# Kernel optimization log

Hardware: AMD Instinct MI355X
Metric: run time of the kernel (lower is better)

The kernel has to match this reference:

```python
import jax, jax.numpy as jnp
import numpy as np

B, S, D = 2, 2048, 1024
H, HD = 16, 64
SCALE = HD ** -0.5  # applied TWICE (q pre-scale + inference score scale), matching the source


def setup_inputs() -> dict:
    key = jax.random.key(0)
    ks = jax.random.split(key, 6)
    std = 0.02
    return {
        "x": jax.random.normal(ks[0], (B, S, D), dtype=jnp.float32),
        "Wq": jax.random.normal(ks[1], (D, D), dtype=jnp.float32) * std,
        "Wk": jax.random.normal(ks[2], (D, D), dtype=jnp.float32) * std,
        "Wv": jax.random.normal(ks[3], (D, D), dtype=jnp.float32) * std,
        "Wo": jax.random.normal(ks[4], (D, D), dtype=jnp.float32) * std,
        "bo": jnp.zeros((D,), dtype=jnp.float32),
    }


def reference(x, Wq, Wk, Wv, Wo, bo):
    b, s, d = x.shape
    # nn.Linear: y = x @ W^T ; split heads: b s (h hd) -> b h s hd
    def split_heads(y):
        return y.reshape(b, s, H, HD).transpose(0, 2, 1, 3)

    q = split_heads(x @ Wq.T) * SCALE          # forward pre-scales q
    k = split_heads(x @ Wk.T)
    v = split_heads(x @ Wv.T)

    # inference path scales scores by SCALE again (double scaling, faithful)
    scores = jnp.einsum("bhsd,bhtd->bhst", q, k) * SCALE  # [B,H,S,S]
    causal = jnp.triu(jnp.full((s, s), -jnp.inf, dtype=scores.dtype), k=1)
    scores = scores + causal[None, None]

    # explicit stable softmax as in the source
    m = jnp.max(scores, axis=-1, keepdims=True)
    e = jnp.exp(scores - m)
    attn = e / jnp.sum(e, axis=-1, keepdims=True)

    out = jnp.einsum("bhst,bhtd->bhsd", attn, v)          # [B,H,S,HD]
    out = out.transpose(0, 2, 1, 3).reshape(b, s, d)       # b h s hd -> b s (h hd)
    return out @ Wo.T + bo
```

## Files before the change

kernel.cpp:

```cpp
#include <hip/hip_runtime.h>
#include <stdint.h>

#define S_LEN 2048
#define DMODEL 1024
#define NHEAD 16
#define HDIM 64
#define BATCH 2

typedef float f32x4 __attribute__((ext_vector_type(4)));
typedef __bf16 bf16x8 __attribute__((ext_vector_type(8)));

typedef const void __attribute__((address_space(1)))* as1_cvp;
typedef void __attribute__((address_space(3)))* as3_vp;

__device__ __forceinline__ ushort f2bf(float f) {
    union { float f; unsigned u; } v; v.f = f;
    unsigned u = v.u;
    return (ushort)((u + 0x7fffu + ((u >> 16) & 1u)) >> 16);
}

__device__ __forceinline__ void gload16(const void* g, void* l) {
    __builtin_amdgcn_global_load_lds((as1_cvp)g, (as3_vp)l, 16, 0, 0);
}

__global__ __launch_bounds__(256) void cvt_all(
    const float* __restrict__ x,  const float* __restrict__ wq,
    const float* __restrict__ wk, const float* __restrict__ wv,
    const float* __restrict__ wo,
    ushort* __restrict__ xb, ushort* __restrict__ wqkv, ushort* __restrict__ wob,
    float qscale) {
    const float* src; ushort* dst; int n; float sc = 1.0f;
    const int DD = DMODEL * DMODEL;
    switch (blockIdx.y) {
        case 0: src = x;  dst = xb;            n = BATCH * S_LEN * DMODEL; break;
        case 1: src = wq; dst = wqkv;          n = DD; sc = qscale; break;
        case 2: src = wk; dst = wqkv + DD;     n = DD; break;
        case 3: src = wv; dst = wqkv + 2 * DD; n = DD; break;
        default: src = wo; dst = wob;          n = DD; break;
    }
    const int step = gridDim.x * 256 * 8;
    for (int i = (blockIdx.x * 256 + threadIdx.x) * 8; i < n; i += step) {
        float4 a = *(const float4*)(src + i);
        float4 b = *(const float4*)(src + i + 4);
        union { ushort us[8]; int4 v; } r;
        r.us[0] = f2bf(a.x * sc); r.us[1] = f2bf(a.y * sc);
        r.us[2] = f2bf(a.z * sc); r.us[3] = f2bf(a.w * sc);
        r.us[4] = f2bf(b.x * sc); r.us[5] = f2bf(b.y * sc);
        r.us[6] = f2bf(b.z * sc); r.us[7] = f2bf(b.w * sc);
        *(int4*)(dst + i) = r.v;
    }
}

template<int BM, int BN, bool F32OUT, bool BIAS>
__global__ __launch_bounds__(256) void gemm_nt(
    const ushort* __restrict__ A, const ushort* __restrict__ B,
    void* __restrict__ Cv, const float* __restrict__ bias,
    int M, int N, int K) {
    __shared__ ushort As[3][BM][32];
    __shared__ ushort Bs[3][BN][32];
    constexpr int MR = BM / 32, NR = BN / 32, AG = BM / 64, BG = BN / 64;
    const int tid = threadIdx.x;
    const int wave = tid >> 6, lane = tid & 63;
    const int wm = (wave >> 1) * (BM / 2), wn = (wave & 1) * (BN / 2);
    const int bm = blockIdx.x * BM, bn = blockIdx.y * BN;
    const int l15 = lane & 15, lg = lane >> 4;
    f32x4 acc[MR][NR] = {};

    const int sr = lane >> 2;
    const int ssw = (((lane & 3) ^ ((lane >> 3) & 3))) * 8;
    const ushort* gA[AG]; const ushort* gB[BG];
    int rA0[AG], rB0[BG];
#pragma unroll
    for (int i = 0; i < AG; i++) {
        rA0[i] = wave * (BM / 4) + i * 16;
        gA[i] = A + (size_t)(bm + rA0[i] + sr) * K + ssw;
    }
#pragma unroll
    for (int i = 0; i < BG; i++) {
        rB0[i] = wave * (BN / 4) + i * 16;
        gB[i] = B + (size_t)(bn + rB0[i] + sr) * K + ssw;
    }

    const int NT = K / 32;
    auto STAGE = [&](int t) {
        const int buf = t % 3;
        const int off = t * 32;
#pragma unroll
        for (int i = 0; i < AG; i++) gload16(gA[i] + off, &As[buf][rA0[i]][0]);
#pragma unroll
        for (int i = 0; i < BG; i++) gload16(gB[i] + off, &Bs[buf][rB0[i]][0]);
    };

    STAGE(0);
    if (NT > 1) STAGE(1);
    asm volatile("s_waitcnt vmcnt(4)" ::: "memory");
    asm volatile("s_barrier" ::: "memory");

    const int csA = (l15 >> 1) & 3;
    for (int t = 0; t < NT; t++) {
        const int cur = t % 3;
        if (t + 2 < NT) STAGE(t + 2);
        bf16x8 af[MR], bfr[NR];
#pragma unroll
        for (int m = 0; m < MR; m++) {
            int4 t_ = *(const int4*)&As[cur][wm + m * 16 + l15][(lg ^ csA) * 8];
            af[m] = __builtin_bit_cast(bf16x8, t_);
        }
#pragma unroll
        for (int n = 0; n < NR; n++) {
            int4 t_ = *(const int4*)&Bs[cur][wn + n * 16 + l15][(lg ^ csA) * 8];
            bfr[n] = __builtin_bit_cast(bf16x8, t_);
        }
        __builtin_amdgcn_s_setprio(1);
#pragma unroll
        for (int m = 0; m < MR; m++)
#pragma unroll
            for (int n = 0; n < NR; n++)
                acc[m][n] = __builtin_amdgcn_mfma_f32_16x16x32_bf16(af[m], bfr[n], acc[m][n], 0, 0, 0);
        __builtin_amdgcn_s_setprio(0);
        if (t + 1 < NT) {
            if (t + 2 < NT) asm volatile("s_waitcnt vmcnt(4)" ::: "memory");
            else            asm volatile("s_waitcnt vmcnt(0)" ::: "memory");
            asm volatile("s_barrier" ::: "memory");
        }
    }

    float* Cf = (float*)Cv;
    ushort* Cb = (ushort*)Cv;
#pragma unroll
    for (int m = 0; m < MR; m++) {
        const int row = bm + wm + m * 16 + lg * 4;
#pragma unroll
        for (int n = 0; n < NR; n++) {
            const int col = bn + wn + n * 16 + l15;
            const float bb = BIAS ? bias[col] : 0.0f;
#pragma unroll
            for (int j = 0; j < 4; j++) {
                float v = acc[m][n][j];
                if (F32OUT) Cf[(size_t)(row + j) * N + col] = v + bb;
                else        Cb[(size_t)(row + j) * N + col] = f2bf(v);
            }
        }
    }
}

__global__ __launch_bounds__(256) void attn_fwd(
    const ushort* __restrict__ QKV, ushort* __restrict__ Og) {
    __shared__ ushort Ks[2][64][72];
    __shared__ ushort Vt[2][64][72];
    __shared__ ushort Ps[4][16][76];
    const int tid = threadIdx.x;
    const int wave = tid >> 6, lane = tid & 63;
    const int l15 = lane & 15, lg = lane >> 4;
    const int a = blockIdx.x;
    const int qtS = a, qtB = 31 - a;
    const int bh = blockIdx.y;
    const int b = bh >> 4, h = bh & 15;
    const ushort* Qb = QKV + (size_t)b * S_LEN * 3072 + h * HDIM;
    const ushort* Kb = Qb + 1024;
    const ushort* Vb = Qb + 2048;

    const int4 onesi = {0x3F803F80, 0x3F803F80, 0x3F803F80, 0x3F803F80};
    const bf16x8 ones = __builtin_bit_cast(bf16x8, onesi);

    bf16x8 qfS[2], qfB[2];
#pragma unroll
    for (int kk = 0; kk < 2; kk++) {
        int4 tS = *(const int4*)(Qb + (size_t)(qtS * 64 + wave * 16 + l15) * 3072 + kk * 32 + lg * 8);
        qfS[kk] = __builtin_bit_cast(bf16x8, tS);
        int4 tB = *(const int4*)(Qb + (size_t)(qtB * 64 + wave * 16 + l15) * 3072 + kk * 32 + lg * 8);
        qfB[kk] = __builtin_bit_cast(bf16x8, tB);
    }

    f32x4 oS[4] = {}, oB[4] = {};
    f32x4 lS = {}, lB = {};

    const int kr = tid >> 2, kc = (tid & 3) * 8;
    const int vt_ = tid & 63, vh = (tid >> 6) * 8;
    int4 kreg0, kreg1, vreg0, vreg1;

    auto LOAD = [&](int t) {
        const ushort* kp = Kb + (size_t)(t * 64 + kr) * 3072 + kc;
        kreg0 = *(const int4*)kp;
        kreg1 = *(const int4*)(kp + 32);
        const ushort* vp = Vb + (size_t)(t * 64 + vt_) * 3072 + vh;
        vreg0 = *(const int4*)vp;
        vreg1 = *(const int4*)(vp + 32);
    };
    auto STORE = [&](int buf) {
        *(int4*)&Ks[buf][kr][kc]      = kreg0;
        *(int4*)&Ks[buf][kr][kc + 32] = kreg1;
        union { int4 v; ushort us[8]; } u0, u1;
        u0.v = vreg0; u1.v = vreg1;
#pragma unroll
        for (int j = 0; j < 8; j++) Vt[buf][vh + j][vt_] = u0.us[j];
#pragma unroll
        for (int j = 0; j < 8; j++) Vt[buf][32 + vh + j][vt_] = u1.us[j];
    };

    auto COMPUTE = [&](const bf16x8 (&qf)[2], f32x4 (&o)[4], f32x4& lacc,
                       bool diag, int cur) {
        f32x4 s[4] = {};
        __builtin_amdgcn_s_setprio(1);
#pragma unroll
        for (int kk = 0; kk < 2; kk++) {
#pragma unroll
            for (int n = 0; n < 4; n++) {
                int4 t = *(const int4*)&Ks[cur][n * 16 + l15][kk * 32 + lg * 8];
                s[n] = __builtin_amdgcn_mfma_f32_16x16x32_bf16(qf[kk], __builtin_bit_cast(bf16x8, t), s[n], 0, 0, 0);
            }
        }
        __builtin_amdgcn_s_setprio(0);
        if (diag) {
            const int qrow = wave * 16 + lg * 4;
#pragma unroll
            for (int n = 0; n < 4; n++) {
                const int tg = n * 16 + l15;
#pragma unroll
                for (int j = 0; j < 4; j++)
                    if (tg > qrow + j) s[n][j] = -1e30f;
            }
        }
#pragma unroll
        for (int n = 0; n < 4; n++)
#pragma unroll
            for (int j = 0; j < 4; j++)
                Ps[wave][lg * 4 + j][n * 16 + l15] = f2bf(__expf(s[n][j]));
        asm volatile("s_waitcnt lgkmcnt(0)" ::: "memory");
        __builtin_amdgcn_s_setprio(1);
#pragma unroll
        for (int kk = 0; kk < 2; kk++) {
            int4 tp = *(const int4*)&Ps[wave][l15][kk * 32 + lg * 8];
            bf16x8 pf = __builtin_bit_cast(bf16x8, tp);
#pragma unroll
            for (int n = 0; n < 4; n++) {
                int4 tv = *(const int4*)&Vt[cur][n * 16 + l15][kk * 32 + lg * 8];
                o[n] = __builtin_amdgcn_mfma_f32_16x16x32_bf16(pf, __builtin_bit_cast(bf16x8, tv), o[n], 0, 0, 0);
            }
            lacc = __builtin_amdgcn_mfma_f32_16x16x32_bf16(pf, ones, lacc, 0, 0, 0);
        }
        __builtin_amdgcn_s_setprio(0);
    };

    LOAD(0);
    STORE(0);
    __syncthreads();

    for (int t0 = 0; t0 <= qtB; ++t0) {
        const int cur = t0 & 1;
        if (t0 < qtB) LOAD(t0 + 1);
        COMPUTE(qfB, oB, lB, t0 == qtB, cur);
        if (t0 <= qtS) COMPUTE(qfS, oS, lS, t0 == qtS, cur);
        if (t0 < qtB) {
            STORE(cur ^ 1);
            __syncthreads();
        }
    }

#pragma unroll
    for (int j = 0; j < 4; j++) { lS[j] = 1.0f / lS[j]; lB[j] = 1.0f / lB[j]; }
#pragma unroll
    for (int n = 0; n < 4; n++)
#pragma unroll
        for (int j = 0; j < 4; j++) {
            const int qrS = qtS * 64 + wave * 16 + lg * 4 + j;
            Og[((size_t)(b * S_LEN + qrS)) * DMODEL + h * HDIM + n * 16 + l15] = f2bf(oS[n][j] * lS[j]);
            const int qrB = qtB * 64 + wave * 16 + lg * 4 + j;
            Og[((size_t)(b * S_LEN + qrB)) * DMODEL + h * HDIM + n * 16 + l15] = f2bf(oB[n][j] * lB[j]);
        }
}

extern "C" void kernel_launch(void* const* d_in, const int* in_sizes, int n_in,
                              void* d_out, int out_size, void* d_ws, size_t ws_size,
                              hipStream_t stream) {
    (void)in_sizes; (void)n_in; (void)out_size; (void)ws_size;
    const float* x  = (const float*)d_in[0];
    const float* Wq = (const float*)d_in[1];
    const float* Wk = (const float*)d_in[2];
    const float* Wv = (const float*)d_in[3];
    const float* Wo = (const float*)d_in[4];
    const float* bo = (const float*)d_in[5];
    float* out = (float*)d_out;

    const int M = BATCH * S_LEN;
    const int D = DMODEL;

    char* ws = (char*)d_ws;
    ushort* xb   = (ushort*)ws; ws += (size_t)M * D * 2;
    ushort* wqkv = (ushort*)ws; ws += (size_t)3 * D * D * 2;
    ushort* wob  = (ushort*)ws; ws += (size_t)D * D * 2;
    ushort* qkvb = (ushort*)ws; ws += (size_t)M * 3 * D * 2;
    ushort* ao   = (ushort*)ws; ws += (size_t)M * D * 2;

    const float qscale = 1.0f / 64.0f;
    cvt_all<<<dim3(512, 5), 256, 0, stream>>>(x, Wq, Wk, Wv, Wo, xb, wqkv, wob, qscale);

    gemm_nt<128, 128, false, false><<<dim3(M / 128, 3 * D / 128), 256, 0, stream>>>(
        xb, wqkv, qkvb, nullptr, M, 3 * D, D);

    attn_fwd<<<dim3(16, BATCH * NHEAD), 256, 0, stream>>>(qkvb, ao);

    gemm_nt<64, 128, true, true><<<dim3(M / 64, D / 128), 256, 0, stream>>>(
        ao, wob, out, bo, M, D, D);
}
```

Measured before the change: 197.4 us.

## Unroll GEMM triple buffer, drop LDS swizzle, one query tile per attention block

The GEMM now uses three named LDS buffers with a manually unrolled 3-stage loop and a templated wait+barrier helper, and it drops the XOR swizzle on LDS reads and writes. The attention kernel no longer pairs a small and a large query tile per block. It launches one block per (query tile, batch-head) on a 1D grid, heaviest tiles first, to get more parallelism and let the scheduler balance load. The risks are more LDS bank conflicts from removing the swizzle, and more K/V reloads with lower per-block reuse. The GEMM tail assumes NT mod 3 == 2, which holds for K=1024.

```diff
diff --git a/kernel.cpp b/kernel.cpp
--- a/kernel.cpp
+++ b/kernel.cpp
@@ -21,6 +21,14 @@
 
 __device__ __forceinline__ void gload16(const void* g, void* l) {
     __builtin_amdgcn_global_load_lds((as1_cvp)g, (as3_vp)l, 16, 0, 0);
+}
+
+template<int N> __device__ __forceinline__ void wait_vm_barrier() {
+    if constexpr (N == 0)      asm volatile("s_waitcnt vmcnt(0)" ::: "memory");
+    else if constexpr (N == 3) asm volatile("s_waitcnt vmcnt(3)" ::: "memory");
+    else if constexpr (N == 4) asm volatile("s_waitcnt vmcnt(4)" ::: "memory");
+    else                       asm volatile("s_waitcnt vmcnt(0)" ::: "memory");
+    asm volatile("s_barrier" ::: "memory");
 }
 
 __global__ __launch_bounds__(256) void cvt_all(
@@ -56,9 +64,10 @@
     const ushort* __restrict__ A, const ushort* __restrict__ B,
     void* __restrict__ Cv, const float* __restrict__ bias,
     int M, int N, int K) {
-    __shared__ ushort As[3][BM][32];
-    __shared__ ushort Bs[3][BN][32];
+    __shared__ ushort As0[BM][32], As1[BM][32], As2[BM][32];
+    __shared__ ushort Bs0[BN][32], Bs1[BN][32], Bs2[BN][32];
     constexpr int MR = BM / 32, NR = BN / 32, AG = BM / 64, BG = BN / 64;
+    constexpr int LPS = AG + BG;
     const int tid = threadIdx.x;
     const int wave = tid >> 6, lane = tid & 63;
     const int wm = (wave >> 1) * (BM / 2), wn = (wave & 1) * (BN / 2);
@@ -66,49 +75,37 @@
     const int l15 = lane & 15, lg = lane >> 4;
     f32x4 acc[MR][NR] = {};
 
-    const int sr = lane >> 2;
-    const int ssw = (((lane & 3) ^ ((lane >> 3) & 3))) * 8;
+    const int sr = lane >> 2, scol = (lane & 3) * 8;
     const ushort* gA[AG]; const ushort* gB[BG];
     int rA0[AG], rB0[BG];
 #pragma unroll
     for (int i = 0; i < AG; i++) {
         rA0[i] = wave * (BM / 4) + i * 16;
-        gA[i] = A + (size_t)(bm + rA0[i] + sr) * K + ssw;
+        gA[i] = A + (size_t)(bm + rA0[i] + sr) * K + scol;
     }
 #pragma unroll
     for (int i = 0; i < BG; i++) {
         rB0[i] = wave * (BN / 4) + i * 16;
-        gB[i] = B + (size_t)(bn + rB0[i] + sr) * K + ssw;
-    }
-
-    const int NT = K / 32;
-    auto STAGE = [&](int t) {
-        const int buf = t % 3;
+        gB[i] = B + (size_t)(bn + rB0[i] + sr) * K + scol;
+    }
+
+    auto STAGE = [&](int t, ushort (*as)[32], ushort (*bs)[32]) {
         const int off = t * 32;
 #pragma unroll
-        for (int i = 0; i < AG; i++) gload16(gA[i] + off, &As[buf][rA0[i]][0]);
-#pragma unroll
-        for (int i = 0; i < BG; i++) gload16(gB[i] + off, &Bs[buf][rB0[i]][0]);
-    };
-
-    STAGE(0);
-    if (NT > 1) STAGE(1);
-    asm volatile("s_waitcnt vmcnt(4)" ::: "memory");
-    asm volatile("s_barrier" ::: "memory");
-
-    const int csA = (l15 >> 1) & 3;
-    for (int t = 0; t < NT; t++) {
-        const int cur = t % 3;
-        if (t + 2 < NT) STAGE(t + 2);
+        for (int i = 0; i < AG; i++) gload16(gA[i] + off, &as[rA0[i]][0]);
+#pragma unroll
+        for (int i = 0; i < BG; i++) gload16(gB[i] + off, &bs[rB0[i]][0]);
+    };
+    auto COMPUTE = [&](ushort (*as)[32], ushort (*bs)[32]) {
         bf16x8 af[MR], bfr[NR];
 #pragma unroll
         for (int m = 0; m < MR; m++) {
-            int4 t_ = *(const int4*)&As[cur][wm + m * 16 + l15][(lg ^ csA) * 8];
+            int4 t_ = *(const int4*)&as[wm + m * 16 + l15][lg * 8];
             af[m] = __builtin_bit_cast(bf16x8, t_);
         }
 #pragma unroll
         for (int n = 0; n < NR; n++) {
-            int4 t_ = *(const int4*)&Bs[cur][wn + n * 16 + l15][(lg ^ csA) * 8];
+            int4 t_ = *(const int4*)&bs[wn + n * 16 + l15][lg * 8];
             bfr[n] = __builtin_bit_cast(bf16x8, t_);
         }
         __builtin_amdgcn_s_setprio(1);
@@ -118,12 +115,22 @@
             for (int n = 0; n < NR; n++)
                 acc[m][n] = __builtin_amdgcn_mfma_f32_16x16x32_bf16(af[m], bfr[n], acc[m][n], 0, 0, 0);
         __builtin_amdgcn_s_setprio(0);
-        if (t + 1 < NT) {
-            if (t + 2 < NT) asm volatile("s_waitcnt vmcnt(4)" ::: "memory");
-            else            asm volatile("s_waitcnt vmcnt(0)" ::: "memory");
-            asm volatile("s_barrier" ::: "memory");
-        }
-    }
+    };
+
+    const int NT = K / 32;
+    STAGE(0, As0, Bs0);
+    STAGE(1, As1, Bs1);
+    wait_vm_barrier<LPS>();
+
+    int t = 0;
+    for (; t + 5 <= NT; t += 3) {
+        STAGE(t + 2, As2, Bs2); COMPUTE(As0, Bs0); wait_vm_barrier<LPS>();
+        STAGE(t + 3, As0, Bs0); COMPUTE(As1, Bs1); wait_vm_barrier<LPS>();
+        STAGE(t + 4, As1, Bs1); COMPUTE(As2, Bs2); wait_vm_barrier<LPS>();
+    }
+    COMPUTE(As0, Bs0);
+    wait_vm_barrier<0>();
+    COMPUTE(As1, Bs1);
 
     float* Cf = (float*)Cv;
     ushort* Cb = (ushort*)Cv;
@@ -152,10 +159,10 @@
     const int tid = threadIdx.x;
     const int wave = tid >> 6, lane = tid & 63;
     const int l15 = lane & 15, lg = lane >> 4;
-    const int a = blockIdx.x;
-    const int qtS = a, qtB = 31 - a;
-    const int bh = blockIdx.y;
+    const int qt = 31 - (blockIdx.x >> 5);
+    const int bh = blockIdx.x & 31;
     const int b = bh >> 4, h = bh & 15;
+    const int q0 = qt * 64;
     const ushort* Qb = QKV + (size_t)b * S_LEN * 3072 + h * HDIM;
     const ushort* Kb = Qb + 1024;
     const ushort* Vb = Qb + 2048;
@@ -163,17 +170,15 @@
     const int4 onesi = {0x3F803F80, 0x3F803F80, 0x3F803F80, 0x3F803F80};
     const bf16x8 ones = __builtin_bit_cast(bf16x8, onesi);
 
-    bf16x8 qfS[2], qfB[2];
+    bf16x8 qf[2];
 #pragma unroll
     for (int kk = 0; kk < 2; kk++) {
-        int4 tS = *(const int4*)(Qb + (size_t)(qtS * 64 + wave * 16 + l15) * 3072 + kk * 32 + lg * 8);
-        qfS[kk] = __builtin_bit_cast(bf16x8, tS);
-        int4 tB = *(const int4*)(Qb + (size_t)(qtB * 64 + wave * 16 + l15) * 3072 + kk * 32 + lg * 8);
-        qfB[kk] = __builtin_bit_cast(bf16x8, tB);
-    }
-
-    f32x4 oS[4] = {}, oB[4] = {};
-    f32x4 lS = {}, lB = {};
+        int4 t = *(const int4*)(Qb + (size_t)(q0 + wave * 16 + l15) * 3072 + kk * 32 + lg * 8);
+        qf[kk] = __builtin_bit_cast(bf16x8, t);
+    }
+
+    f32x4 o[4] = {};
+    f32x4 lacc = {};
 
     const int kr = tid >> 2, kc = (tid & 3) * 8;
     const int vt_ = tid & 63, vh = (tid >> 6) * 8;
@@ -198,8 +203,7 @@
         for (int j = 0; j < 8; j++) Vt[buf][32 + vh + j][vt_] = u1.us[j];
     };
 
-    auto COMPUTE = [&](const bf16x8 (&qf)[2], f32x4 (&o)[4], f32x4& lacc,
-                       bool diag, int cur) {
+    auto COMPUTE = [&](bool diag, int cur) {
         f32x4 s[4] = {};
         __builtin_amdgcn_s_setprio(1);
 #pragma unroll
@@ -246,27 +250,24 @@
     STORE(0);
     __syncthreads();
 
-    for (int t0 = 0; t0 <= qtB; ++t0) {
+    for (int t0 = 0; t0 <= qt; ++t0) {
         const int cur = t0 & 1;
-        if (t0 < qtB) LOAD(t0 + 1);
-        COMPUTE(qfB, oB, lB, t0 == qtB, cur);
-        if (t0 <= qtS) COMPUTE(qfS, oS, lS, t0 == qtS, cur);
-        if (t0 < qtB) {
+        if (t0 < qt) LOAD(t0 + 1);
+        COMPUTE(t0 == qt, cur);
+        if (t0 < qt) {
             STORE(cur ^ 1);
             __syncthreads();
         }
     }
 
 #pragma unroll
-    for (int j = 0; j < 4; j++) { lS[j] = 1.0f / lS[j]; lB[j] = 1.0f / lB[j]; }
+    for (int j = 0; j < 4; j++) lacc[j] = 1.0f / lacc[j];
 #pragma unroll
     for (int n = 0; n < 4; n++)
 #pragma unroll
         for (int j = 0; j < 4; j++) {
-            const int qrS = qtS * 64 + wave * 16 + lg * 4 + j;
-            Og[((size_t)(b * S_LEN + qrS)) * DMODEL + h * HDIM + n * 16 + l15] = f2bf(oS[n][j] * lS[j]);
-            const int qrB = qtB * 64 + wave * 16 + lg * 4 + j;
-            Og[((size_t)(b * S_LEN + qrB)) * DMODEL + h * HDIM + n * 16 + l15] = f2bf(oB[n][j] * lB[j]);
+            const int qrow = q0 + wave * 16 + lg * 4 + j;
+            Og[((size_t)(b * S_LEN + qrow)) * DMODEL + h * HDIM + n * 16 + l15] = f2bf(o[n][j] * lacc[j]);
         }
 }
 
@@ -298,7 +299,7 @@
     gemm_nt<128, 128, false, false><<<dim3(M / 128, 3 * D / 128), 256, 0, stream>>>(
         xb, wqkv, qkvb, nullptr, M, 3 * D, D);
 
-    attn_fwd<<<dim3(16, BATCH * NHEAD), 256, 0, stream>>>(qkvb, ao);
+    attn_fwd<<<dim3(32 * BATCH * NHEAD), 256, 0, stream>>>(qkvb, ao);
 
     gemm_nt<64, 128, true, true><<<dim3(M / 64, D / 128), 256, 0, stream>>>(
         ao, wob, out, bo, M, D, D);
```

Measured after the change: 191.0 us. -3.2%, faster.
